# Kernel tuning notes

Hardware: AMD Instinct MI355X
Metric: run time of the kernel (lower is better)

Reference implementation:

```python
import jax, jax.numpy as jnp
import numpy as np

N = 100000
E = 3200000
IN_DIM = 256
HID = 128
OUT_DIM = 64


def setup_inputs() -> dict:
    key = jax.random.key(0)
    ks = jax.random.split(key, 8)
    features = jax.random.normal(ks[0], (N, IN_DIM), dtype=jnp.float32)
    edge_row = jax.random.randint(ks[1], (E,), 0, N, dtype=jnp.int32)
    edge_col = jax.random.randint(ks[2], (E,), 0, N, dtype=jnp.int32)
    edge_val = jax.random.uniform(ks[3], (E,), dtype=jnp.float32)
    W1 = jax.random.normal(ks[4], (IN_DIM, HID), dtype=jnp.float32) * (1.0 / np.sqrt(IN_DIM))
    b1 = jnp.zeros((HID,), dtype=jnp.float32)
    W2 = jax.random.normal(ks[5], (HID, OUT_DIM), dtype=jnp.float32) * (1.0 / np.sqrt(HID))
    b2 = jnp.zeros((OUT_DIM,), dtype=jnp.float32)
    return {"features": features, "edge_row": edge_row, "edge_col": edge_col,
            "edge_val": edge_val, "W1": W1, "b1": b1, "W2": W2, "b2": b2}


def reference(features, edge_row, edge_col, edge_val, W1, b1, W2, b2):
    # fc1: [N, IN_DIM] @ [IN_DIM, HID] + b1
    h = features @ W1 + b1                                   # [N, HID]
    # spmm(A, h): for each edge (r, c, v): out[r] += v * h[c]
    msgs = edge_val[:, None] * h[edge_col]                    # [E, HID] gather
    h = jax.ops.segment_sum(msgs, edge_row, num_segments=N)   # [N, HID] scatter-add
    h = jax.nn.relu(h)
    h = h @ W2 + b2                                           # [N, OUT_DIM]
    return jax.nn.log_softmax(h, axis=1)
```

## Files before the change

### kernel.cpp

```cpp
#include <hip/hip_runtime.h>
#include <math.h>

constexpr int IN_DIM  = 256;
constexpr int HID     = 128;
constexpr int OUT_DIM = 64;

constexpr int BROWS   = 128;
constexpr int NBUCK   = 782;
constexpr int CAP     = 4608;
constexpr int CAP2    = 5504;
constexpr int CHUNK2  = 2048;
constexpr int GC_STRIDE = 16;

typedef short  bf16x8 __attribute__((ext_vector_type(8)));
typedef float  f32x4  __attribute__((ext_vector_type(4)));
typedef float  f32x2  __attribute__((ext_vector_type(2)));
typedef int    i32x4  __attribute__((ext_vector_type(4)));

__device__ __forceinline__ unsigned short f2bf(float x) {
    union { float f; unsigned u; } v; v.f = x;
    unsigned r = v.u + 0x7FFF + ((v.u >> 16) & 1);
    return (unsigned short)(r >> 16);
}

__global__ __launch_bounds__(256) void wt_kernel(const float* __restrict__ W1,
                                                 unsigned short* __restrict__ W1T)
{
    int idx = blockIdx.x * 256 + threadIdx.x;
    int k = idx >> 7;
    int n = idx & 127;
    W1T[n * IN_DIM + k] = f2bf(W1[idx]);
}

__global__ __launch_bounds__(256) void fc1_bin_fused(
        const float* __restrict__ feat,
        const unsigned short* __restrict__ W1T,
        const float* __restrict__ b1,
        unsigned short* __restrict__ h1b, int N,
        const int* __restrict__ erow,
        const int* __restrict__ ecol,
        const float* __restrict__ eval,
        int* __restrict__ gCursor,
        int2* __restrict__ binned, int E)
{
    __shared__ int sCnt[NBUCK];
    __shared__ int sBase[NBUCK];

    const int nfc1 = (N + 63) >> 6;
    const int nbin = (E + CHUNK2 - 1) / CHUNK2;
    const int nInter = 2 * min(nfc1, nbin);
    const int b = blockIdx.x;

    bool isBin;
    int  id;
    if (b < nInter) { isBin = (b & 1); id = b >> 1; }
    else            { isBin = (nbin > nfc1); id = min(nfc1, nbin) + (b - nInter); }

    const int t = threadIdx.x;

    if (!isBin) {
        const int lane = t & 63;
        const int w    = t >> 6;
        const int quad = lane >> 4;
        const int ln15 = lane & 15;
        const int row0 = id * 64;

        int arow = row0 + w * 16 + ln15;
        if (arow >= N) arow = N - 1;
        const float* aptr = feat + (size_t)arow * IN_DIM + quad * 8;

        f32x4 acc[8];
#pragma unroll
        for (int i = 0; i < 8; ++i) acc[i] = (f32x4){0.f, 0.f, 0.f, 0.f};

#pragma unroll
        for (int ks = 0; ks < 8; ++ks) {
            float4 a0 = *(const float4*)(aptr + ks * 32);
            float4 a1 = *(const float4*)(aptr + ks * 32 + 4);
            bf16x8 afrag;
            afrag[0] = (short)f2bf(a0.x); afrag[1] = (short)f2bf(a0.y);
            afrag[2] = (short)f2bf(a0.z); afrag[3] = (short)f2bf(a0.w);
            afrag[4] = (short)f2bf(a1.x); afrag[5] = (short)f2bf(a1.y);
            afrag[6] = (short)f2bf(a1.z); afrag[7] = (short)f2bf(a1.w);
#pragma unroll
            for (int nt = 0; nt < 8; ++nt) {
                bf16x8 bfrag = *(const bf16x8*)&W1T[(size_t)(nt * 16 + ln15) * IN_DIM + ks * 32 + quad * 8];
                acc[nt] = __builtin_amdgcn_mfma_f32_16x16x32_bf16(afrag, bfrag, acc[nt], 0, 0, 0);
            }
        }

#pragma unroll
        for (int nt = 0; nt < 8; ++nt) {
            int col = nt * 16 + ln15;
            float bias = b1[col];
#pragma unroll
            for (int r = 0; r < 4; ++r) {
                int grow = row0 + w * 16 + quad * 4 + r;
                if (grow < N)
                    h1b[(size_t)grow * HID + col] = f2bf(acc[nt][r] + bias);
            }
        }
    } else {
        const int e0   = id * CHUNK2;
        const int eEnd = min(e0 + CHUNK2, E);

        for (int i = t; i < NBUCK; i += 256) sCnt[i] = 0;
        __syncthreads();

        for (int e = e0 + t; e < eEnd; e += 256)
            atomicAdd(&sCnt[erow[e] >> 7], 1);
        __syncthreads();

        for (int i = t; i < NBUCK; i += 256) {
            int c = sCnt[i];
            sBase[i] = c ? atomicAdd(&gCursor[i * GC_STRIDE], c) : 0;
            sCnt[i] = 0;
        }
        __syncthreads();

        for (int e = e0 + t; e < eEnd; e += 256) {
            int   r = erow[e];
            int   c = ecol[e];
            float v = eval[e];
            int   bk = r >> 7;
            int off = sBase[bk] + atomicAdd(&sCnt[bk], 1);
            if (off < CAP)
                binned[(size_t)bk * CAP + off] = make_int2((c << 8) | ((r & 127) << 25),
                                                           __float_as_int(v));
        }
    }
}

__global__ __launch_bounds__(256) void sort_bucket4(const int* __restrict__ gCursor,
                                                    const int2* __restrict__ binned,
                                                    int2* __restrict__ edges2,
                                                    int2* __restrict__ rowIdx, int N)
{
    __shared__ int2 sE[CAP];
    __shared__ int sHist[BROWS];
    __shared__ int sStart[BROWS + 1];
    __shared__ int sCur[BROWS];
    const int t  = threadIdx.x;
    const int b  = blockIdx.x;
    const int nE = min(gCursor[b * GC_STRIDE], CAP);
    const size_t baseIn  = (size_t)b * CAP;
    const size_t baseOut = (size_t)b * CAP2;

    if (t < BROWS) sHist[t] = 0;
    __syncthreads();

    for (int i = t; i < nE; i += 256) {
        int2 p = binned[baseIn + i];
        sE[i] = p;
        atomicAdd(&sHist[(unsigned)p.x >> 25], 1);
    }
    __syncthreads();

    if (t < BROWS) sStart[t + 1] = (sHist[t] + 7) & ~7;
    if (t == 0) sStart[0] = 0;
    __syncthreads();
    for (int o = 1; o < BROWS; o <<= 1) {
        int v = 0;
        if (t < BROWS) {
            v = sStart[t + 1];
            if (t >= o) v += sStart[t + 1 - o];
        }
        __syncthreads();
        if (t < BROWS) sStart[t + 1] = v;
        __syncthreads();
    }
    if (t < BROWS) sCur[t] = sStart[t];
    __syncthreads();

    for (int i = t; i < nE; i += 256) {
        int2 p = sE[i];
        int rl = (unsigned)p.x >> 25;
        int pos = atomicAdd(&sCur[rl], 1);
        edges2[baseOut + pos] = p;
    }

    if (t < BROWS) {
        int h  = sHist[t];
        int ph = (h + 7) & ~7;
        size_t p0 = baseOut + sStart[t];
        for (int k = h; k < ph; ++k)
            edges2[p0 + k] = make_int2(0, 0);
        int rr = b * BROWS + t;
        if (rr < N)
            rowIdx[rr] = make_int2((int)p0, (int)(p0 + ph));
    }
}

__global__ __launch_bounds__(512) void spmm_fc2(const int2* __restrict__ rowIdx,
                                                const int2* __restrict__ edges2,
                                                const unsigned short* __restrict__ h1b,
                                                const float* __restrict__ W2,
                                                const float* __restrict__ b2,
                                                float* __restrict__ out, int N)
{
    __shared__ __align__(16) float sW2[HID * OUT_DIM];
    __shared__ float sH2[8][HID];
    const int t    = threadIdx.x;
    const int lane = t & 63;
    const int wv   = t >> 6;

#pragma unroll
    for (int i = 0; i < 4; ++i) {
        int f = i * 512 + t;
        *(float4*)&sW2[f * 4] = *(const float4*)&W2[f * 4];
    }
    __syncthreads();

    const int r = blockIdx.x * 8 + wv;
    float ax = 0.f, ay = 0.f;

    if (r < N) {
        const int lane4 = lane * 4;
        const char* h1base = (const char*)h1b;
        const int2 se = rowIdx[r];
        int j = se.x;
        const int jend = se.y;
        f32x2 acc = (f32x2){0.f, 0.f};

        for (; j + 16 <= jend; j += 16) {
            i32x4 q[8];
#pragma unroll
            for (int u = 0; u < 8; ++u)
                q[u] = __builtin_nontemporal_load((const i32x4*)&edges2[j + u * 2]);
            unsigned g[16];
#pragma unroll
            for (int u = 0; u < 8; ++u) {
                g[2 * u]     = *(const unsigned*)(h1base + (q[u].x & 0x01FFFFFF) + lane4);
                g[2 * u + 1] = *(const unsigned*)(h1base + (q[u].z & 0x01FFFFFF) + lane4);
            }
#pragma unroll
            for (int u = 0; u < 8; ++u) {
                f32x2 h0 = (f32x2){__uint_as_float(g[2 * u] << 16),
                                   __uint_as_float(g[2 * u] & 0xFFFF0000u)};
                f32x2 h1 = (f32x2){__uint_as_float(g[2 * u + 1] << 16),
                                   __uint_as_float(g[2 * u + 1] & 0xFFFF0000u)};
                acc += h0 * __int_as_float(q[u].y);
                acc += h1 * __int_as_float(q[u].w);
            }
        }
        if (j < jend) {
            i32x4 q[4];
#pragma unroll
            for (int u = 0; u < 4; ++u)
                q[u] = __builtin_nontemporal_load((const i32x4*)&edges2[j + u * 2]);
            unsigned g[8];
#pragma unroll
            for (int u = 0; u < 4; ++u) {
                g[2 * u]     = *(const unsigned*)(h1base + (q[u].x & 0x01FFFFFF) + lane4);
                g[2 * u + 1] = *(const unsigned*)(h1base + (q[u].z & 0x01FFFFFF) + lane4);
            }
#pragma unroll
            for (int u = 0; u < 4; ++u) {
                f32x2 h0 = (f32x2){__uint_as_float(g[2 * u] << 16),
                                   __uint_as_float(g[2 * u] & 0xFFFF0000u)};
                f32x2 h1 = (f32x2){__uint_as_float(g[2 * u + 1] << 16),
                                   __uint_as_float(g[2 * u + 1] & 0xFFFF0000u)};
                acc += h0 * __int_as_float(q[u].y);
                acc += h1 * __int_as_float(q[u].w);
            }
        }
        ax = fmaxf(acc.x, 0.f);
        ay = fmaxf(acc.y, 0.f);
    }

    sH2[wv][lane * 2]     = ax;
    sH2[wv][lane * 2 + 1] = ay;

    if (r < N) {
        float acc = b2[lane];
        const float* w2l = &sW2[lane];
#pragma unroll 8
        for (int k = 0; k < HID; ++k)
            acc = fmaf(sH2[wv][k], w2l[k * OUT_DIM], acc);

        float m = acc;
#pragma unroll
        for (int o = 1; o < 64; o <<= 1) m = fmaxf(m, __shfl_xor(m, o));
        float e = __expf(acc - m);
        float s = e;
#pragma unroll
        for (int o = 1; o < 64; o <<= 1) s += __shfl_xor(s, o);

        out[(size_t)r * OUT_DIM + lane] = acc - m - __logf(s);
    }
}

extern "C" void kernel_launch(void* const* d_in, const int* in_sizes, int n_in,
                              void* d_out, int out_size, void* d_ws, size_t ws_size,
                              hipStream_t stream) {
    const float* feat = (const float*)d_in[0];
    const int*   erow = (const int*)d_in[1];
    const int*   ecol = (const int*)d_in[2];
    const float* eval = (const float*)d_in[3];
    const float* W1   = (const float*)d_in[4];
    const float* b1   = (const float*)d_in[5];
    const float* W2   = (const float*)d_in[6];
    const float* b2   = (const float*)d_in[7];
    float*       out  = (float*)d_out;

    const int N = in_sizes[0] / IN_DIM;
    const int E = in_sizes[1];

    unsigned short* h1b    = (unsigned short*)d_ws;
    int2*           binned = (int2*)(h1b + (size_t)N * HID);
    int2*           edges2 = binned + (size_t)NBUCK * CAP;
    int2*           rowIdx = edges2 + (size_t)NBUCK * CAP2;
    unsigned short* W1T    = (unsigned short*)(rowIdx + N);
    int*            gCursor= (int*)(W1T + IN_DIM * HID);

    hipMemsetAsync(gCursor, 0, NBUCK * GC_STRIDE * sizeof(int), stream);

    wt_kernel<<<(IN_DIM * HID) / 256, 256, 0, stream>>>(W1, W1T);

    const int nfc1 = (N + 63) / 64;
    const int nbin = (E + CHUNK2 - 1) / CHUNK2;
    fc1_bin_fused<<<nfc1 + nbin, 256, 0, stream>>>(feat, W1T, b1, h1b, N,
                                                   erow, ecol, eval,
                                                   gCursor, binned, E);

    sort_bucket4<<<NBUCK, 256, 0, stream>>>(gCursor, binned, edges2, rowIdx, N);

    const int nblk = (N + 7) / 8;
    spmm_fc2<<<nblk, 512, 0, stream>>>(rowIdx, edges2, h1b, W2, b2, out, N);
}
```

Before: 464.6 us.

## Split fused fc1/binning kernel, stage W1 in LDS, fold cursor memset

The interleaved fc1+binning kernel is split into separate kernels. fc1 now uses 512-thread blocks covering 128 rows and stages the whole bf16 W1 (re-laid-out for conflict-free fragment reads) into LDS via global_load_lds instead of reading it from global memory per MFMA. The binning kernel uses 1024-thread blocks with larger edge chunks, which means fewer global cursor atomics. The gCursor memset is folded into the weight-transpose kernel. The cost is that fc1 and binning no longer overlap in a single launch, and each fc1 block uses 64KB of LDS, which limits occupancy.

After: 434.4 us. -6.5%, faster.

```diff
diff --git a/kernel.cpp b/kernel.cpp
--- a/kernel.cpp
+++ b/kernel.cpp
@@ -9,7 +9,7 @@
 constexpr int NBUCK   = 782;
 constexpr int CAP     = 4608;
 constexpr int CAP2    = 5504;
-constexpr int CHUNK2  = 2048;
+constexpr int CHUNK   = 8192;
 constexpr int GC_STRIDE = 16;
 
 typedef short  bf16x8 __attribute__((ext_vector_type(8)));
@@ -23,111 +23,119 @@
     return (unsigned short)(r >> 16);
 }
 
+__device__ __forceinline__ void load_lds16(const void* g, void* l) {
+    __builtin_amdgcn_global_load_lds(
+        (const __attribute__((address_space(1))) unsigned int*)g,
+        (__attribute__((address_space(3))) unsigned int*)l, 16, 0, 0);
+}
+
 __global__ __launch_bounds__(256) void wt_kernel(const float* __restrict__ W1,
-                                                 unsigned short* __restrict__ W1T)
+                                                 unsigned short* __restrict__ W1T2,
+                                                 int* __restrict__ gCursor)
 {
     int idx = blockIdx.x * 256 + threadIdx.x;
     int k = idx >> 7;
     int n = idx & 127;
-    W1T[n * IN_DIM + k] = f2bf(W1[idx]);
-}
-
-__global__ __launch_bounds__(256) void fc1_bin_fused(
-        const float* __restrict__ feat,
-        const unsigned short* __restrict__ W1T,
-        const float* __restrict__ b1,
-        unsigned short* __restrict__ h1b, int N,
-        const int* __restrict__ erow,
-        const int* __restrict__ ecol,
-        const float* __restrict__ eval,
-        int* __restrict__ gCursor,
-        int2* __restrict__ binned, int E)
+    W1T2[(k >> 3) * 1024 + n * 8 + (k & 7)] = f2bf(W1[idx]);
+
+    if (idx < NBUCK * GC_STRIDE)
+        gCursor[idx] = 0;
+}
+
+__global__ __launch_bounds__(512, 4) void fc1_mfma(const float* __restrict__ feat,
+                                                   const unsigned short* __restrict__ W1T2,
+                                                   const float* __restrict__ b1,
+                                                   unsigned short* __restrict__ h1b, int N)
+{
+    __shared__ unsigned short sW1[IN_DIM * HID];
+    const int t    = threadIdx.x;
+    const int lane = t & 63;
+    const int w    = t >> 6;
+    const int quad = lane >> 4;
+    const int ln15 = lane & 15;
+    const int row0 = blockIdx.x * 128;
+
+#pragma unroll
+    for (int i = 0; i < 8; ++i) {
+        int off = i * 4096 + w * 512;
+        load_lds16(W1T2 + off + lane * 8, &sW1[off]);
+    }
+    __syncthreads();
+
+    int arow = row0 + w * 16 + ln15;
+    if (arow >= N) arow = N - 1;
+    const float* aptr = feat + (size_t)arow * IN_DIM + quad * 8;
+
+    f32x4 acc[8];
+#pragma unroll
+    for (int i = 0; i < 8; ++i) acc[i] = (f32x4){0.f, 0.f, 0.f, 0.f};
+
+#pragma unroll
+    for (int ks = 0; ks < 8; ++ks) {
+        float4 a0 = *(const float4*)(aptr + ks * 32);
+        float4 a1 = *(const float4*)(aptr + ks * 32 + 4);
+        bf16x8 afrag;
+        afrag[0] = (short)f2bf(a0.x); afrag[1] = (short)f2bf(a0.y);
+        afrag[2] = (short)f2bf(a0.z); afrag[3] = (short)f2bf(a0.w);
+        afrag[4] = (short)f2bf(a1.x); afrag[5] = (short)f2bf(a1.y);
+        afrag[6] = (short)f2bf(a1.z); afrag[7] = (short)f2bf(a1.w);
+
+        const unsigned short* bbase = &sW1[(ks * 4 + quad) * 1024 + ln15 * 8];
+#pragma unroll
+        for (int nt = 0; nt < 8; ++nt) {
+            bf16x8 bfrag = *(const bf16x8*)(bbase + nt * 128);
+            acc[nt] = __builtin_amdgcn_mfma_f32_16x16x32_bf16(afrag, bfrag, acc[nt], 0, 0, 0);
+        }
+    }
+
+#pragma unroll
+    for (int nt = 0; nt < 8; ++nt) {
+        int col = nt * 16 + ln15;
+        float bias = b1[col];
+#pragma unroll
+        for (int r = 0; r < 4; ++r) {
+            int grow = row0 + w * 16 + quad * 4 + r;
+            if (grow < N)
+                h1b[(size_t)grow * HID + col] = f2bf(acc[nt][r] + bias);
+        }
+    }
+}
+
+__global__ __launch_bounds__(1024) void bin_kernel(const int* __restrict__ erow,
+                                                   const int* __restrict__ ecol,
+                                                   const float* __restrict__ eval,
+                                                   int* __restrict__ gCursor,
+                                                   int2* __restrict__ binned, int E)
 {
     __shared__ int sCnt[NBUCK];
     __shared__ int sBase[NBUCK];
-
-    const int nfc1 = (N + 63) >> 6;
-    const int nbin = (E + CHUNK2 - 1) / CHUNK2;
-    const int nInter = 2 * min(nfc1, nbin);
-    const int b = blockIdx.x;
-
-    bool isBin;
-    int  id;
-    if (b < nInter) { isBin = (b & 1); id = b >> 1; }
-    else            { isBin = (nbin > nfc1); id = min(nfc1, nbin) + (b - nInter); }
-
     const int t = threadIdx.x;
-
-    if (!isBin) {
-        const int lane = t & 63;
-        const int w    = t >> 6;
-        const int quad = lane >> 4;
-        const int ln15 = lane & 15;
-        const int row0 = id * 64;
-
-        int arow = row0 + w * 16 + ln15;
-        if (arow >= N) arow = N - 1;
-        const float* aptr = feat + (size_t)arow * IN_DIM + quad * 8;
-
-        f32x4 acc[8];
-#pragma unroll
-        for (int i = 0; i < 8; ++i) acc[i] = (f32x4){0.f, 0.f, 0.f, 0.f};
-
-#pragma unroll
-        for (int ks = 0; ks < 8; ++ks) {
-            float4 a0 = *(const float4*)(aptr + ks * 32);
-            float4 a1 = *(const float4*)(aptr + ks * 32 + 4);
-            bf16x8 afrag;
-            afrag[0] = (short)f2bf(a0.x); afrag[1] = (short)f2bf(a0.y);
-            afrag[2] = (short)f2bf(a0.z); afrag[3] = (short)f2bf(a0.w);
-            afrag[4] = (short)f2bf(a1.x); afrag[5] = (short)f2bf(a1.y);
-            afrag[6] = (short)f2bf(a1.z); afrag[7] = (short)f2bf(a1.w);
-#pragma unroll
-            for (int nt = 0; nt < 8; ++nt) {
-                bf16x8 bfrag = *(const bf16x8*)&W1T[(size_t)(nt * 16 + ln15) * IN_DIM + ks * 32 + quad * 8];
-                acc[nt] = __builtin_amdgcn_mfma_f32_16x16x32_bf16(afrag, bfrag, acc[nt], 0, 0, 0);
-            }
-        }
-
-#pragma unroll
-        for (int nt = 0; nt < 8; ++nt) {
-            int col = nt * 16 + ln15;
-            float bias = b1[col];
-#pragma unroll
-            for (int r = 0; r < 4; ++r) {
-                int grow = row0 + w * 16 + quad * 4 + r;
-                if (grow < N)
-                    h1b[(size_t)grow * HID + col] = f2bf(acc[nt][r] + bias);
-            }
-        }
-    } else {
-        const int e0   = id * CHUNK2;
-        const int eEnd = min(e0 + CHUNK2, E);
-
-        for (int i = t; i < NBUCK; i += 256) sCnt[i] = 0;
-        __syncthreads();
-
-        for (int e = e0 + t; e < eEnd; e += 256)
-            atomicAdd(&sCnt[erow[e] >> 7], 1);
-        __syncthreads();
-
-        for (int i = t; i < NBUCK; i += 256) {
-            int c = sCnt[i];
-            sBase[i] = c ? atomicAdd(&gCursor[i * GC_STRIDE], c) : 0;
-            sCnt[i] = 0;
-        }
-        __syncthreads();
-
-        for (int e = e0 + t; e < eEnd; e += 256) {
-            int   r = erow[e];
-            int   c = ecol[e];
-            float v = eval[e];
-            int   bk = r >> 7;
-            int off = sBase[bk] + atomicAdd(&sCnt[bk], 1);
-            if (off < CAP)
-                binned[(size_t)bk * CAP + off] = make_int2((c << 8) | ((r & 127) << 25),
-                                                           __float_as_int(v));
-        }
+    const int e0 = blockIdx.x * CHUNK;
+    const int eEnd = min(e0 + CHUNK, E);
+
+    for (int i = t; i < NBUCK; i += 1024) sCnt[i] = 0;
+    __syncthreads();
+
+    for (int e = e0 + t; e < eEnd; e += 1024)
+        atomicAdd(&sCnt[erow[e] >> 7], 1);
+    __syncthreads();
+
+    for (int i = t; i < NBUCK; i += 1024) {
+        int c = sCnt[i];
+        sBase[i] = c ? atomicAdd(&gCursor[i * GC_STRIDE], c) : 0;
+        sCnt[i] = 0;
+    }
+    __syncthreads();
+
+    for (int e = e0 + t; e < eEnd; e += 1024) {
+        int   r = erow[e];
+        int   c = ecol[e];
+        float v = eval[e];
+        int   b = r >> 7;
+        int off = sBase[b] + atomicAdd(&sCnt[b], 1);
+        if (off < CAP)
+            binned[(size_t)b * CAP + off] = make_int2((c << 8) | ((r & 127) << 25),
+                                                      __float_as_int(v));
     }
 }
 
@@ -310,21 +318,17 @@
     int2*           binned = (int2*)(h1b + (size_t)N * HID);
     int2*           edges2 = binned + (size_t)NBUCK * CAP;
     int2*           rowIdx = edges2 + (size_t)NBUCK * CAP2;
-    unsigned short* W1T    = (unsigned short*)(rowIdx + N);
-    int*            gCursor= (int*)(W1T + IN_DIM * HID);
-
-    hipMemsetAsync(gCursor, 0, NBUCK * GC_STRIDE * sizeof(int), stream);
-
-    wt_kernel<<<(IN_DIM * HID) / 256, 256, 0, stream>>>(W1, W1T);
-
-    const int nfc1 = (N + 63) / 64;
-    const int nbin = (E + CHUNK2 - 1) / CHUNK2;
-    fc1_bin_fused<<<nfc1 + nbin, 256, 0, stream>>>(feat, W1T, b1, h1b, N,
-                                                   erow, ecol, eval,
-                                                   gCursor, binned, E);
+    unsigned short* W1T2   = (unsigned short*)(rowIdx + N);
+    int*            gCursor= (int*)(W1T2 + IN_DIM * HID);
+
+    wt_kernel<<<(IN_DIM * HID) / 256, 256, 0, stream>>>(W1, W1T2, gCursor);
+
+    fc1_mfma<<<(N + 127) / 128, 512, 0, stream>>>(feat, W1T2, b1, h1b, N);
+
+    bin_kernel<<<(E + CHUNK - 1) / CHUNK, 1024, 0, stream>>>(erow, ecol, eval,
+                                                             gCursor, binned, E);
 
     sort_bucket4<<<NBUCK, 256, 0, stream>>>(gCursor, binned, edges2, rowIdx, N);
 
-    const int nblk = (N + 7) / 8;
-    spmm_fc2<<<nblk, 512, 0, stream>>>(rowIdx, edges2, h1b, W2, b2, out, N);
-}
+    spmm_fc2<<<(N + 7) / 8, 512, 0, stream>>>(rowIdx, edges2, h1b, W2, b2, out, N);
+}
```
